# Kernel tuning notes

Hardware: AMD Instinct MI355X
Metric: run time of the kernel (lower is better)

The kernel has to match this reference:

```python
import jax, jax.numpy as jnp
import numpy as np

N, F, UNITS = 8192, 512, 128
EDGE_PROB = 0.004  # ~32 neighbors per node
NEG_INF = -1e10


def setup_inputs() -> dict:
    key = jax.random.key(0)
    ks = jax.random.split(key, 7)
    features = jax.random.normal(ks[0], (N, F), dtype=jnp.float32)
    A = (jax.random.uniform(ks[1], (N, N)) < EDGE_PROB).astype(jnp.float32)
    kernel = jax.random.normal(ks[2], (UNITS, F), dtype=jnp.float32) * (1.0 / np.sqrt(F))
    a_self = jax.random.normal(ks[3], (UNITS, 1), dtype=jnp.float32) * (1.0 / np.sqrt(UNITS))
    a_cross = jax.random.normal(ks[4], (UNITS, 1), dtype=jnp.float32) * (1.0 / np.sqrt(UNITS))
    dense_w = jax.random.normal(ks[5], (UNITS, UNITS), dtype=jnp.float32) * (1.0 / np.sqrt(UNITS))
    dense_b = jnp.zeros((UNITS,), dtype=jnp.float32)
    return {"features": features, "A": A, "kernel": kernel, "a_self": a_self,
            "a_cross": a_cross, "dense_w": dense_w, "dense_b": dense_b}


def reference(features, A, kernel, a_self, a_cross, dense_w, dense_b):
    # feature transform: [N, F] @ [F, units] -> [N, units]
    ft = features @ kernel.T
    s = ft @ a_self    # [N, 1]
    c = ft @ a_cross   # [N, 1]
    att = s + c.T      # [N, N] pairwise scores
    scores = jax.nn.leaky_relu(att, negative_slope=0.2)
    masked = scores + NEG_INF * (1.0 - A)
    sm = jax.nn.softmax(masked, axis=0)  # column-wise softmax (axis=0, as in TF code)
    out = sm @ ft                        # [N, units]
    # Flatten on [N, units] is identity; final Dense(units)
    return out @ dense_w + dense_b
```

## Files before the change

### kernel.cpp

```cpp
#include <hip/hip_runtime.h>
#include <math.h>


#define NND 8192
#define FFD 512
#define UUD 128
#define CAP 128

typedef float f32x4 __attribute__((ext_vector_type(4)));

__global__ __launch_bounds__(256) void k_ft(const float* __restrict__ feat,
                                            const float* __restrict__ ker,
                                            const float* __restrict__ a_self,
                                            const float* __restrict__ a_cross,
                                            float* __restrict__ ft,
                                            float* __restrict__ s,
                                            float* __restrict__ c) {
    __shared__ float As[32][36];
    __shared__ float Bs[32][132];
    const int tid = threadIdx.x;
    const int r0 = blockIdx.x * 32;
    const int tc = tid & 31;
    const int tr = tid >> 5;
    float acc[4][4];
#pragma unroll
    for (int x = 0; x < 4; x++)
#pragma unroll
        for (int y = 0; y < 4; y++) acc[x][y] = 0.f;

    for (int k0 = 0; k0 < FFD; k0 += 32) {
        __syncthreads();
        {
            int r = tid >> 3;
            int k4 = (tid & 7) << 2;
            f32x4 v = *(const f32x4*)&feat[(size_t)(r0 + r) * FFD + k0 + k4];
            As[k4 + 0][r] = v[0]; As[k4 + 1][r] = v[1];
            As[k4 + 2][r] = v[2]; As[k4 + 3][r] = v[3];
        }
#pragma unroll
        for (int it = 0; it < 4; it++) {
            int u = it * 32 + (tid >> 3);
            int k4 = (tid & 7) << 2;
            f32x4 v = *(const f32x4*)&ker[(size_t)u * FFD + k0 + k4];
            Bs[k4 + 0][u] = v[0]; Bs[k4 + 1][u] = v[1];
            Bs[k4 + 2][u] = v[2]; Bs[k4 + 3][u] = v[3];
        }
        __syncthreads();
#pragma unroll
        for (int kk = 0; kk < 32; kk++) {
            f32x4 a = *(const f32x4*)&As[kk][tr << 2];
            f32x4 b = *(const f32x4*)&Bs[kk][tc << 2];
#pragma unroll
            for (int x = 0; x < 4; x++)
#pragma unroll
                for (int y = 0; y < 4; y++) acc[x][y] += a[x] * b[y];
        }
    }
#pragma unroll
    for (int x = 0; x < 4; x++) {
        int i = r0 + (tr << 2) + x;
        f32x4 v; v[0] = acc[x][0]; v[1] = acc[x][1]; v[2] = acc[x][2]; v[3] = acc[x][3];
        *(f32x4*)&ft[(size_t)i * UUD + (tc << 2)] = v;
    }

    f32x4 asv = *(const f32x4*)&a_self[tc << 2];
    f32x4 acv = *(const f32x4*)&a_cross[tc << 2];
#pragma unroll
    for (int x = 0; x < 4; x++) {
        float sv = acc[x][0] * asv[0] + acc[x][1] * asv[1] + acc[x][2] * asv[2] + acc[x][3] * asv[3];
        float cv = acc[x][0] * acv[0] + acc[x][1] * acv[1] + acc[x][2] * acv[2] + acc[x][3] * acv[3];
#pragma unroll
        for (int off = 16; off; off >>= 1) {
            sv += __shfl_xor(sv, off);
            cv += __shfl_xor(cv, off);
        }
        if (tc == 0) {
            int i = r0 + (tr << 2) + x;
            s[i] = sv; c[i] = cv;
        }
    }
}

__global__ __launch_bounds__(256) void k_scan(const float* __restrict__ A,
                                              const float* __restrict__ s,
                                              const float* __restrict__ c,
                                              int* __restrict__ row_cnt,
                                              int* __restrict__ edge_j,
                                              float* __restrict__ edge_w,
                                              float* __restrict__ denom) {
    __shared__ int cnt;
    const int i = blockIdx.x;
    const int tid = threadIdx.x;
    if (tid == 0) cnt = 0;
    __syncthreads();
    const float si = s[i];
    const f32x4* A4 = (const f32x4*)&A[(size_t)i * NND];
    for (int it = 0; it < 8; it++) {
        int idx = it * 256 + tid;
        f32x4 v = __builtin_nontemporal_load(&A4[idx]);
#pragma unroll
        for (int m = 0; m < 4; m++) {
            if (v[m] != 0.f) {
                int j = (idx << 2) + m;
                float sc = si + c[j];
                sc = fmaxf(sc, 0.2f * sc);
                float w = expf(sc);
                int pos = atomicAdd(&cnt, 1);
                if (pos < CAP) {
                    edge_j[i * CAP + pos] = j;
                    edge_w[i * CAP + pos] = w;
                }
                atomicAdd(&denom[j], w);
            }
        }
    }
    __syncthreads();
    if (tid == 0) row_cnt[i] = (cnt < CAP) ? cnt : CAP;
}

__global__ __launch_bounds__(256) void k_z(const float* __restrict__ denom,
                                           const float* __restrict__ ft,
                                           float* __restrict__ zsum,
                                           int* __restrict__ zflag) {
    int j = blockIdx.x * 256 + threadIdx.x;
    if (denom[j] == 0.f) {
        atomicAdd(zflag, 1);
        for (int u = 0; u < UUD; u++) atomicAdd(&zsum[u], ft[(size_t)j * UUD + u]);
    }
}

__global__ __launch_bounds__(256) void k_agg_out(const int* __restrict__ row_cnt,
                                                 const int* __restrict__ edge_j,
                                                 const float* __restrict__ edge_w,
                                                 const float* __restrict__ denom,
                                                 const float* __restrict__ ft,
                                                 const float* __restrict__ zsum,
                                                 const int* __restrict__ zflag,
                                                 const float* __restrict__ W,
                                                 const float* __restrict__ bias,
                                                 float* __restrict__ out) {
    __shared__ float rowbuf[4][128];
    const int wv = threadIdx.x >> 6;
    const int lane = threadIdx.x & 63;
    const int i = blockIdx.x * 4 + wv;
    const int cnt = row_cnt[i];
    float acc0 = 0.f, acc1 = 0.f;
#pragma unroll 4
    for (int e = 0; e < cnt; e++) {
        int j = edge_j[i * CAP + e];
        float w = edge_w[i * CAP + e] / denom[j];
        acc0 += w * ft[(size_t)j * UUD + lane];
        acc1 += w * ft[(size_t)j * UUD + 64 + lane];
    }
    if (*zflag) {
        const float invN = 1.f / (float)NND;
        acc0 += invN * zsum[lane];
        acc1 += invN * zsum[64 + lane];
    }
    rowbuf[wv][lane] = acc0;
    rowbuf[wv][64 + lane] = acc1;
    __syncthreads();
    float o0 = bias[lane], o1 = bias[64 + lane];
    for (int v = 0; v < UUD; v += 4) {
        f32x4 rv = *(const f32x4*)&rowbuf[wv][v];
#pragma unroll
        for (int mm = 0; mm < 4; mm++) {
            o0 += rv[mm] * W[(size_t)(v + mm) * UUD + lane];
            o1 += rv[mm] * W[(size_t)(v + mm) * UUD + 64 + lane];
        }
    }
    out[(size_t)i * UUD + lane] = o0;
    out[(size_t)i * UUD + 64 + lane] = o1;
}

extern "C" void kernel_launch(void* const* d_in, const int* in_sizes, int n_in,
                              void* d_out, int out_size, void* d_ws, size_t ws_size,
                              hipStream_t stream) {
    const float* feat    = (const float*)d_in[0];
    const float* A       = (const float*)d_in[1];
    const float* ker     = (const float*)d_in[2];
    const float* a_self  = (const float*)d_in[3];
    const float* a_cross = (const float*)d_in[4];
    const float* W       = (const float*)d_in[5];
    const float* bias    = (const float*)d_in[6];
    float* out = (float*)d_out;

    char* p = (char*)d_ws;
    float* ft      = (float*)p;  p += (size_t)NND * UUD * 4;
    int*   edge_j  = (int*)p;    p += (size_t)NND * CAP * 4;
    float* edge_w  = (float*)p;  p += (size_t)NND * CAP * 4;
    float* s       = (float*)p;  p += NND * 4;
    float* c       = (float*)p;  p += NND * 4;
    int*   row_cnt = (int*)p;    p += NND * 4;
    float* denom   = (float*)p;  p += NND * 4;
    float* zsum    = (float*)p;  p += UUD * 4;
    int*   zflag   = (int*)p;    p += 4;

    hipMemsetAsync(denom, 0, (NND + UUD + 1) * 4, stream);

    k_ft<<<NND / 32, 256, 0, stream>>>(feat, ker, a_self, a_cross, ft, s, c);
    k_scan<<<NND, 256, 0, stream>>>(A, s, c, row_cnt, edge_j, edge_w, denom);
    k_z<<<NND / 256, 256, 0, stream>>>(denom, ft, zsum, zflag);
    k_agg_out<<<NND / 4, 256, 0, stream>>>(row_cnt, edge_j, edge_w, denom, ft,
                                           zsum, zflag, W, bias, out);
}
```

Measured before the change: 434.1 us.

## Halve GEMM row tile, batch A-row loads, split aggregation across two waves

The feature-transform GEMM now computes 16 rows per block instead of 32, giving 512 blocks for better CU occupancy at the cost of reloading the kernel tile more often. The adjacency scan issues all eight nontemporal row loads up front so the memory requests overlap. The aggregation kernel stages normalized edge weights and indices in shared memory, splits each row's edges across two wavefronts, and adds a reduction step. The output dense product is also spread across 128 threads per row.

```diff
diff --git a/kernel.cpp b/kernel.cpp
--- a/kernel.cpp
+++ b/kernel.cpp
@@ -16,21 +16,21 @@
                                             float* __restrict__ ft,
                                             float* __restrict__ s,
                                             float* __restrict__ c) {
-    __shared__ float As[32][36];
+    __shared__ float As[32][20];
     __shared__ float Bs[32][132];
     const int tid = threadIdx.x;
-    const int r0 = blockIdx.x * 32;
+    const int r0 = blockIdx.x * 16;
     const int tc = tid & 31;
     const int tr = tid >> 5;
-    float acc[4][4];
-#pragma unroll
-    for (int x = 0; x < 4; x++)
+    float acc[2][4];
+#pragma unroll
+    for (int x = 0; x < 2; x++)
 #pragma unroll
         for (int y = 0; y < 4; y++) acc[x][y] = 0.f;
 
     for (int k0 = 0; k0 < FFD; k0 += 32) {
         __syncthreads();
-        {
+        if (tid < 128) {
             int r = tid >> 3;
             int k4 = (tid & 7) << 2;
             f32x4 v = *(const f32x4*)&feat[(size_t)(r0 + r) * FFD + k0 + k4];
@@ -48,17 +48,19 @@
         __syncthreads();
 #pragma unroll
         for (int kk = 0; kk < 32; kk++) {
-            f32x4 a = *(const f32x4*)&As[kk][tr << 2];
+            float a0 = As[kk][(tr << 1) + 0];
+            float a1 = As[kk][(tr << 1) + 1];
             f32x4 b = *(const f32x4*)&Bs[kk][tc << 2];
 #pragma unroll
-            for (int x = 0; x < 4; x++)
-#pragma unroll
-                for (int y = 0; y < 4; y++) acc[x][y] += a[x] * b[y];
-        }
-    }
-#pragma unroll
-    for (int x = 0; x < 4; x++) {
-        int i = r0 + (tr << 2) + x;
+            for (int y = 0; y < 4; y++) {
+                acc[0][y] += a0 * b[y];
+                acc[1][y] += a1 * b[y];
+            }
+        }
+    }
+#pragma unroll
+    for (int x = 0; x < 2; x++) {
+        int i = r0 + (tr << 1) + x;
         f32x4 v; v[0] = acc[x][0]; v[1] = acc[x][1]; v[2] = acc[x][2]; v[3] = acc[x][3];
         *(f32x4*)&ft[(size_t)i * UUD + (tc << 2)] = v;
     }
@@ -66,7 +68,7 @@
     f32x4 asv = *(const f32x4*)&a_self[tc << 2];
     f32x4 acv = *(const f32x4*)&a_cross[tc << 2];
 #pragma unroll
-    for (int x = 0; x < 4; x++) {
+    for (int x = 0; x < 2; x++) {
         float sv = acc[x][0] * asv[0] + acc[x][1] * asv[1] + acc[x][2] * asv[2] + acc[x][3] * asv[3];
         float cv = acc[x][0] * acv[0] + acc[x][1] * acv[1] + acc[x][2] * acv[2] + acc[x][3] * acv[3];
 #pragma unroll
@@ -75,7 +77,7 @@
             cv += __shfl_xor(cv, off);
         }
         if (tc == 0) {
-            int i = r0 + (tr << 2) + x;
+            int i = r0 + (tr << 1) + x;
             s[i] = sv; c[i] = cv;
         }
     }
@@ -95,13 +97,16 @@
     __syncthreads();
     const float si = s[i];
     const f32x4* A4 = (const f32x4*)&A[(size_t)i * NND];
+    f32x4 vv[8];
+#pragma unroll
+    for (int it = 0; it < 8; it++)
+        vv[it] = __builtin_nontemporal_load(&A4[it * 256 + tid]);
+#pragma unroll
     for (int it = 0; it < 8; it++) {
-        int idx = it * 256 + tid;
-        f32x4 v = __builtin_nontemporal_load(&A4[idx]);
 #pragma unroll
         for (int m = 0; m < 4; m++) {
-            if (v[m] != 0.f) {
-                int j = (idx << 2) + m;
+            if (vv[it][m] != 0.f) {
+                int j = ((it * 256 + tid) << 2) + m;
                 float sc = si + c[j];
                 sc = fmaxf(sc, 0.2f * sc);
                 float w = expf(sc);
@@ -139,38 +144,53 @@
                                                  const float* __restrict__ W,
                                                  const float* __restrict__ bias,
                                                  float* __restrict__ out) {
-    __shared__ float rowbuf[4][128];
-    const int wv = threadIdx.x >> 6;
-    const int lane = threadIdx.x & 63;
-    const int i = blockIdx.x * 4 + wv;
+    __shared__ int   jbuf[2][CAP];
+    __shared__ float wbuf[2][CAP];
+    __shared__ float rowpart[2][2][128];
+    __shared__ float rowfull[2][128];
+    const int tid = threadIdx.x;
+    const int wv = tid >> 6;
+    const int lane = tid & 63;
+    const int r = wv >> 1;
+    const int sub = wv & 1;
+    const int i = blockIdx.x * 2 + r;
     const int cnt = row_cnt[i];
+
+    {
+        int e = sub * 64 + lane;
+        if (e < cnt) {
+            int j = edge_j[i * CAP + e];
+            jbuf[r][e] = j;
+            wbuf[r][e] = edge_w[i * CAP + e] / denom[j];
+        }
+    }
+    __syncthreads();
+
     float acc0 = 0.f, acc1 = 0.f;
-#pragma unroll 4
-    for (int e = 0; e < cnt; e++) {
-        int j = edge_j[i * CAP + e];
-        float w = edge_w[i * CAP + e] / denom[j];
+    for (int e = sub; e < cnt; e += 2) {
+        int j = jbuf[r][e];
+        float w = wbuf[r][e];
         acc0 += w * ft[(size_t)j * UUD + lane];
         acc1 += w * ft[(size_t)j * UUD + 64 + lane];
     }
-    if (*zflag) {
-        const float invN = 1.f / (float)NND;
-        acc0 += invN * zsum[lane];
-        acc1 += invN * zsum[64 + lane];
-    }
-    rowbuf[wv][lane] = acc0;
-    rowbuf[wv][64 + lane] = acc1;
-    __syncthreads();
-    float o0 = bias[lane], o1 = bias[64 + lane];
+    rowpart[r][sub][lane] = acc0;
+    rowpart[r][sub][64 + lane] = acc1;
+    __syncthreads();
+
+    const int u = sub * 64 + lane;
+    float agg = rowpart[r][0][u] + rowpart[r][1][u];
+    if (*zflag) agg += (1.f / (float)NND) * zsum[u];
+    rowfull[r][u] = agg;
+    __syncthreads();
+
+    float o = bias[u];
     for (int v = 0; v < UUD; v += 4) {
-        f32x4 rv = *(const f32x4*)&rowbuf[wv][v];
-#pragma unroll
-        for (int mm = 0; mm < 4; mm++) {
-            o0 += rv[mm] * W[(size_t)(v + mm) * UUD + lane];
-            o1 += rv[mm] * W[(size_t)(v + mm) * UUD + 64 + lane];
-        }
-    }
-    out[(size_t)i * UUD + lane] = o0;
-    out[(size_t)i * UUD + 64 + lane] = o1;
+        f32x4 rv = *(const f32x4*)&rowfull[r][v];
+#pragma unroll
+        for (int mm = 0; mm < 4; mm++)
+            o += rv[mm] * W[(size_t)(v + mm) * UUD + u];
+    }
+    out[(size_t)i * UUD + u] = o;
 }
 
 extern "C" void kernel_launch(void* const* d_in, const int* in_sizes, int n_in,
@@ -198,9 +218,9 @@
 
     hipMemsetAsync(denom, 0, (NND + UUD + 1) * 4, stream);
 
-    k_ft<<<NND / 32, 256, 0, stream>>>(feat, ker, a_self, a_cross, ft, s, c);
+    k_ft<<<NND / 16, 256, 0, stream>>>(feat, ker, a_self, a_cross, ft, s, c);
     k_scan<<<NND, 256, 0, stream>>>(A, s, c, row_cnt, edge_j, edge_w, denom);
     k_z<<<NND / 256, 256, 0, stream>>>(denom, ft, zsum, zflag);
-    k_agg_out<<<NND / 4, 256, 0, stream>>>(row_cnt, edge_j, edge_w, denom, ft,
+    k_agg_out<<<NND / 2, 256, 0, stream>>>(row_cnt, edge_j, edge_w, denom, ft,
                                            zsum, zflag, W, bias, out);
 }
```

Measured after the change: 433.8 us. Within noise of the previous version (-0.1%).
